# Performance work log

Measured on AMD Instinct MI355X. Metric: run time of the kernel, lower is better.

## Reference

```python
import jax, jax.numpy as jnp
import numpy as np

N = 50000       # nodes
E = 800000      # edges (before self-loops)
NFEAT = 256
NHID = 64
NHEADS = 4
NOUT = 256
NEG_SLOPE = 0.2
BN_EPS = 1e-5
LN_EPS = 1e-5


def setup_inputs() -> dict:
    key = jax.random.key(0)
    ks = jax.random.split(key, 12)
    g = lambda k, s: (jax.random.normal(k, s, dtype=jnp.float32) * 0.05)
    inp = {
        "x": jax.random.normal(ks[0], (N, NFEAT), dtype=jnp.float32),
        "edge_index": jax.random.randint(ks[1], (2, E), 0, N, dtype=jnp.int32),
        # layer 1: GATConv(NFEAT, NHID, heads=NHEADS, concat=True)
        "W1": g(ks[2], (NFEAT, NHEADS * NHID)),
        "att_src1": g(ks[3], (NHEADS, NHID)),
        "att_dst1": g(ks[4], (NHEADS, NHID)),
        "bias1": jnp.zeros((NHEADS * NHID,), jnp.float32),
        # layer 2: GATConv(NHEADS*NHID, NOUT, heads=1, concat=False)
        "W2": g(ks[5], (NHEADS * NHID, NOUT)),
        "att_src2": g(ks[6], (1, NOUT)),
        "att_dst2": g(ks[7], (1, NOUT)),
        "bias2": jnp.zeros((NOUT,), jnp.float32),
        # BatchNorm1d (eval mode: running stats)
        "bn_gamma": jnp.ones((NOUT,), jnp.float32),
        "bn_beta": jnp.zeros((NOUT,), jnp.float32),
        "bn_mean": g(ks[8], (NOUT,)),
        "bn_var": jnp.ones((NOUT,), jnp.float32),
        # LayerNorm
        "ln_gamma": jnp.ones((NOUT,), jnp.float32),
        "ln_beta": jnp.zeros((NOUT,), jnp.float32),
    }
    return inp


def _gat_conv(x, edge_index, W, att_src, att_dst, bias, concat):
    """PyG-style GATConv (eval mode, add_self_loops=True)."""
    n = x.shape[0]
    H, C = att_src.shape
    xp = (x @ W).reshape(n, H, C)                    # [N,H,C]
    loop = jnp.arange(n, dtype=edge_index.dtype)
    src = jnp.concatenate([edge_index[0], loop])     # message source j
    dst = jnp.concatenate([edge_index[1], loop])     # aggregation target i
    a_src = jnp.einsum("nhc,hc->nh", xp, att_src)    # [N,H]
    a_dst = jnp.einsum("nhc,hc->nh", xp, att_dst)
    e = jax.nn.leaky_relu(a_src[src] + a_dst[dst], NEG_SLOPE)  # [Etot,H]
    # segment softmax over edges sharing the same dst
    m = jax.ops.segment_max(e, dst, num_segments=n)
    e = jnp.exp(e - m[dst])
    denom = jax.ops.segment_sum(e, dst, num_segments=n)
    alpha = e / (denom[dst] + 1e-16)                 # [Etot,H]
    out = jax.ops.segment_sum(alpha[:, :, None] * xp[src], dst, num_segments=n)  # [N,H,C]
    out = out.reshape(n, H * C) if concat else out.mean(axis=1)
    return out + bias


def reference(x, edge_index, W1, att_src1, att_dst1, bias1,
              W2, att_src2, att_dst2, bias2,
              bn_gamma, bn_beta, bn_mean, bn_var, ln_gamma, ln_beta):
    # eval mode: F.dropout is identity
    h = jax.nn.elu(_gat_conv(x, edge_index, W1, att_src1, att_dst1, bias1, True))
    h = jax.nn.elu(_gat_conv(h, edge_index, W2, att_src2, att_dst2, bias2, False))
    # BatchNorm1d (eval: running stats)
    h = (h - bn_mean) * jax.lax.rsqrt(bn_var + BN_EPS) * bn_gamma + bn_beta
    # LayerNorm over last dim
    mu = h.mean(axis=-1, keepdims=True)
    var = jnp.mean((h - mu) ** 2, axis=-1, keepdims=True)
    h = (h - mu) * jax.lax.rsqrt(var + LN_EPS) * ln_gamma + ln_beta
    return h
```

## Files before the change

kernel.cpp:

```cpp
#include <hip/hip_runtime.h>
#include <cstddef>
#include <cstdint>

#define NNODES 50000
#define NEDGES 800000
#define FDIM   256

#define SCAN_BLOCKS 256
#define SCAN_CHUNK  ((NNODES + SCAN_BLOCKS - 1) / SCAN_BLOCKS)

typedef __attribute__((ext_vector_type(8))) _Float16 f16x8;
typedef __attribute__((ext_vector_type(8))) unsigned short ushort8;
typedef __attribute__((ext_vector_type(4))) float f32x4;

__device__ __forceinline__ float leaky_exp(float a) {
    float e = a > 0.f ? a : 0.2f * a;
    return __expf(e);
}
__device__ __forceinline__ unsigned short f2h(float f) {
    return __builtin_bit_cast(unsigned short, (_Float16)f);
}
__device__ __forceinline__ float hlo(uint32_t u) {
    _Float16 h = __builtin_bit_cast(_Float16, (unsigned short)(u & 0xffffu));
    return (float)h;
}
__device__ __forceinline__ float hhi(uint32_t u) {
    _Float16 h = __builtin_bit_cast(_Float16, (unsigned short)(u >> 16));
    return (float)h;
}
__device__ __forceinline__ float rlanef(float v, int l) {
    return __builtin_bit_cast(float,
        __builtin_amdgcn_readlane(__builtin_bit_cast(int, v), l));
}

__global__ __launch_bounds__(256) void cvt_k(const float* __restrict__ in,
                                             unsigned short* __restrict__ out,
                                             int n8) {
    int i = blockIdx.x * 256 + threadIdx.x;
    if (i >= n8) return;
    const float4* p = (const float4*)in + (size_t)i * 2;
    float4 a = p[0], b = p[1];
    ushort8 r;
    r[0] = f2h(a.x); r[1] = f2h(a.y); r[2] = f2h(a.z); r[3] = f2h(a.w);
    r[4] = f2h(b.x); r[5] = f2h(b.y); r[6] = f2h(b.z); r[7] = f2h(b.w);
    *(ushort8*)(out + (size_t)i * 8) = r;
}

__global__ __launch_bounds__(256) void wprep_k(const float* __restrict__ W,
                                               unsigned short* __restrict__ Wt) {
    int n = blockIdx.x, k = threadIdx.x;
    Wt[n * 256 + k] = f2h(W[k * 256 + n]);
}

__global__ __launch_bounds__(256) void gemm_mfma(const unsigned short* __restrict__ A,
                                                 const unsigned short* __restrict__ Bt,
                                                 unsigned short* __restrict__ C, int M) {
    __shared__ unsigned short As[128 * 64];
    __shared__ unsigned short Bs[128 * 64];
    const int t = threadIdx.x;
    const int lane = t & 63, wid = t >> 6;
    const int wr = wid >> 1, wc = wid & 1;
    const int bm = blockIdx.x * 128;
    const int bn = blockIdx.y * 128;
    f32x4 acc[4][4] = {};
    const int lrow = t >> 3, lslot = t & 7;
    for (int k0 = 0; k0 < 256; k0 += 64) {
        __syncthreads();
#pragma unroll
        for (int i = 0; i < 4; ++i) {
            int row = lrow + 32 * i;
            int ga = bm + row; ga = ga < M ? ga : M - 1;
            uint4 av = *(const uint4*)(A + (size_t)ga * FDIM + k0 + lslot * 8);
            *(uint4*)(As + row * 64 + ((lslot ^ (row & 7)) << 3)) = av;
            uint4 bv = *(const uint4*)(Bt + (size_t)(bn + row) * FDIM + k0 + lslot * 8);
            *(uint4*)(Bs + row * 64 + ((lslot ^ (row & 7)) << 3)) = bv;
        }
        __syncthreads();
#pragma unroll
        for (int ks = 0; ks < 2; ++ks) {
            const int kq = ks * 4 + (lane >> 4);
            f16x8 a[4], b[4];
#pragma unroll
            for (int f = 0; f < 4; ++f) {
                int ra = wr * 64 + f * 16 + (lane & 15);
                a[f] = *(const f16x8*)(As + ra * 64 + ((kq ^ (ra & 7)) << 3));
                int rb = wc * 64 + f * 16 + (lane & 15);
                b[f] = *(const f16x8*)(Bs + rb * 64 + ((kq ^ (rb & 7)) << 3));
            }
#pragma unroll
            for (int mf = 0; mf < 4; ++mf)
#pragma unroll
                for (int nf = 0; nf < 4; ++nf)
                    acc[mf][nf] = __builtin_amdgcn_mfma_f32_16x16x32_f16(
                        a[mf], b[nf], acc[mf][nf], 0, 0, 0);
        }
    }
    const int col0 = bn + wc * 64 + (lane & 15);
    const int row00 = bm + wr * 64 + (lane >> 4) * 4;
#pragma unroll
    for (int mf = 0; mf < 4; ++mf)
#pragma unroll
        for (int nf = 0; nf < 4; ++nf) {
            f32x4 v = acc[mf][nf];
            int col = col0 + nf * 16;
#pragma unroll
            for (int r = 0; r < 4; ++r) {
                int row = row00 + mf * 16 + r;
                if (row < M) C[(size_t)row * FDIM + col] = f2h(v[r]);
            }
        }
}

template <int H>
__global__ __launch_bounds__(256) void aprep_k(const unsigned short* __restrict__ xp,
                                               const float* __restrict__ atts,
                                               const float* __restrict__ attd,
                                               float* __restrict__ as_,
                                               float* __restrict__ ad_) {
    const int lane = threadIdx.x & 63;
    const int n = blockIdx.x * 4 + (threadIdx.x >> 6);
    if (n >= NNODES) return;
    const int c = lane << 2;
    uint2 u = *(const uint2*)(xp + (size_t)n * FDIM + c);
    float v0 = hlo(u.x), v1 = hhi(u.x), v2 = hlo(u.y), v3 = hhi(u.y);
    float4 s4 = *(const float4*)(atts + c);
    float4 d4 = *(const float4*)(attd + c);
    float ss = v0 * s4.x + v1 * s4.y + v2 * s4.z + v3 * s4.w;
    float sd = v0 * d4.x + v1 * d4.y + v2 * d4.z + v3 * d4.w;
    constexpr int G = 64 / H;
#pragma unroll
    for (int off = 1; off < G; off <<= 1) {
        ss += __shfl_xor(ss, off);
        sd += __shfl_xor(sd, off);
    }
    if ((lane & (G - 1)) == 0) {
        int h = lane / G;
        as_[n * H + h] = ss;
        ad_[n * H + h] = sd;
    }
}

__global__ __launch_bounds__(256) void hist_k(const int* __restrict__ ei,
                                              int* __restrict__ deg) {
    int e = blockIdx.x * 256 + threadIdx.x;
    if (e < NEDGES) atomicAdd(&deg[ei[NEDGES + e]], 1);
}

__global__ __launch_bounds__(256) void scanA_k(const int* __restrict__ deg,
                                               int* __restrict__ bsum) {
    const int b = blockIdx.x, t = threadIdx.x;
    const int i = b * SCAN_CHUNK + t;
    int v = (t < SCAN_CHUNK && i < NNODES) ? deg[i] : 0;
#pragma unroll
    for (int off = 1; off < 64; off <<= 1) v += __shfl_xor(v, off);
    __shared__ int ws[4];
    if ((t & 63) == 0) ws[t >> 6] = v;
    __syncthreads();
    if (t == 0) bsum[b] = ws[0] + ws[1] + ws[2] + ws[3];
}

__global__ __launch_bounds__(256) void scanB_k(const int* __restrict__ bsum,
                                               int* __restrict__ boff,
                                               int* __restrict__ rowptr) {
    const int t = threadIdx.x;
    const int lane = t & 63, wid = t >> 6;
    int orig = bsum[t];
    int v = orig;
#pragma unroll
    for (int off = 1; off < 64; off <<= 1) {
        int u = __shfl_up(v, off);
        if (lane >= off) v += u;
    }
    __shared__ int ws[4], wo[4];
    if (lane == 63) ws[wid] = v;
    __syncthreads();
    if (t == 0) {
        int a = 0;
        for (int k = 0; k < 4; ++k) { wo[k] = a; a += ws[k]; }
        rowptr[NNODES] = a;
    }
    __syncthreads();
    boff[t] = wo[wid] + v - orig;
}

__global__ __launch_bounds__(256) void scanC_k(const int* __restrict__ deg,
                                               const int* __restrict__ boff,
                                               int* __restrict__ rowptr) {
    const int b = blockIdx.x, t = threadIdx.x;
    const int i = b * SCAN_CHUNK + t;
    const bool ok = (t < SCAN_CHUNK && i < NNODES);
    int orig = ok ? deg[i] : 0;
    int v = orig;
    const int lane = t & 63, wid = t >> 6;
#pragma unroll
    for (int off = 1; off < 64; off <<= 1) {
        int u = __shfl_up(v, off);
        if (lane >= off) v += u;
    }
    __shared__ int ws[4], wo[4];
    if (lane == 63) ws[wid] = v;
    __syncthreads();
    if (t == 0) {
        int a = 0;
        for (int k = 0; k < 4; ++k) { wo[k] = a; a += ws[k]; }
    }
    __syncthreads();
    if (ok) rowptr[i] = boff[b] + wo[wid] + v - orig;
}

__global__ __launch_bounds__(256) void scatter_k(const int* __restrict__ ei,
                                                 const int* __restrict__ rowptr,
                                                 int* __restrict__ deg,
                                                 int* __restrict__ ssrc) {
    int e = blockIdx.x * 256 + threadIdx.x;
    if (e >= NEDGES) return;
    int s = ei[e], d = ei[NEDGES + e];
    int old = atomicSub(&deg[d], 1);
    ssrc[rowptr[d + 1] - old] = s;
}

__global__ __launch_bounds__(256) void gather1_k(const unsigned short* __restrict__ xp,
                                                 const float* __restrict__ as_,
                                                 const float* __restrict__ ad_,
                                                 const int* __restrict__ rowptr,
                                                 const int* __restrict__ ssrc,
                                                 const float* __restrict__ bias,
                                                 unsigned short* __restrict__ out) {
    const int lane = threadIdx.x & 63;
    const int n = blockIdx.x * 4 + (threadIdx.x >> 6);
    if (n >= NNODES) return;
    const int h = lane >> 4;
    const int c = lane << 2;
    const int eloc = lane >> 2;
    const int hh = lane & 3;
    const float adW = ad_[n * 4 + hh];
    float a0 = 0.f, a1 = 0.f, a2 = 0.f, a3 = 0.f, den = 0.f;
    const int beg = rowptr[n], end = rowptr[n + 1];
    for (int base = beg; base < end; base += 16) {
        int my_e = base + eloc;
        float wv = 0.f; int sv = 0;
        if (my_e < end) {
            sv = ssrc[my_e];
            wv = leaky_exp(as_[sv * 4 + hh] + adW);
        }
        float dred = wv;
#pragma unroll
        for (int off = 4; off < 64; off <<= 1) dred += __shfl_xor(dred, off);
        den += __shfl(dred, h);
        const int cnt = min(16, end - base);
        int e = 0;
        for (; e + 8 <= cnt; e += 8) {
            uint2 u[8]; float w[8];
#pragma unroll
            for (int q = 0; q < 8; ++q) {
                int sq = __builtin_amdgcn_readlane(sv, (e + q) << 2);
                u[q] = *(const uint2*)(xp + (((unsigned)sq << 8) + (unsigned)c));
                w[q] = __shfl(wv, ((e + q) << 2) | h);
            }
#pragma unroll
            for (int q = 0; q < 8; ++q) {
                a0 = fmaf(hlo(u[q].x), w[q], a0);
                a1 = fmaf(hhi(u[q].x), w[q], a1);
                a2 = fmaf(hlo(u[q].y), w[q], a2);
                a3 = fmaf(hhi(u[q].y), w[q], a3);
            }
        }
        for (; e < cnt; ++e) {
            int sq = __builtin_amdgcn_readlane(sv, e << 2);
            uint2 u0 = *(const uint2*)(xp + (((unsigned)sq << 8) + (unsigned)c));
            float w0 = __shfl(wv, (e << 2) | h);
            a0 = fmaf(hlo(u0.x), w0, a0); a1 = fmaf(hhi(u0.x), w0, a1);
            a2 = fmaf(hlo(u0.y), w0, a2); a3 = fmaf(hhi(u0.y), w0, a3);
        }
    }
    {
        float w = leaky_exp(as_[n * 4 + h] + ad_[n * 4 + h]);
        uint2 u = *(const uint2*)(xp + (((unsigned)n << 8) + (unsigned)c));
        a0 = fmaf(hlo(u.x), w, a0); a1 = fmaf(hhi(u.x), w, a1);
        a2 = fmaf(hlo(u.y), w, a2); a3 = fmaf(hhi(u.y), w, a3);
        den += w;
    }
    const float inv = 1.f / (den + 1e-16f);
    float4 b4 = *(const float4*)(bias + c);
    float o[4] = {a0 * inv + b4.x, a1 * inv + b4.y,
                  a2 * inv + b4.z, a3 * inv + b4.w};
#pragma unroll
    for (int j = 0; j < 4; ++j) o[j] = o[j] > 0.f ? o[j] : __expf(o[j]) - 1.f;
    ushort4 r;
    r.x = f2h(o[0]); r.y = f2h(o[1]); r.z = f2h(o[2]); r.w = f2h(o[3]);
    *(ushort4*)(out + (size_t)n * FDIM + c) = r;
}

__global__ __launch_bounds__(256) void gather2_k(const unsigned short* __restrict__ xp,
                                                 const float* __restrict__ as_,
                                                 const float* __restrict__ ad_,
                                                 const int* __restrict__ rowptr,
                                                 const int* __restrict__ ssrc,
                                                 const float* __restrict__ bias,
                                                 const float* __restrict__ bng,
                                                 const float* __restrict__ bnb,
                                                 const float* __restrict__ bnm,
                                                 const float* __restrict__ bnv,
                                                 const float* __restrict__ lng,
                                                 const float* __restrict__ lnb,
                                                 float* __restrict__ out) {
    const int lane = threadIdx.x & 63;
    const int n = blockIdx.x * 4 + (threadIdx.x >> 6);
    if (n >= NNODES) return;
    const int c = lane << 2;
    const float adn = ad_[n];
    float a0 = 0.f, a1 = 0.f, a2 = 0.f, a3 = 0.f, den = 0.f;
    const int beg = rowptr[n], end = rowptr[n + 1];
    for (int base = beg; base < end; base += 64) {
        int my_e = base + lane;
        float wv = 0.f; int sv = 0;
        if (my_e < end) {
            sv = ssrc[my_e];
            wv = leaky_exp(as_[sv] + adn);
        }
        float dred = wv;
#pragma unroll
        for (int off = 1; off < 64; off <<= 1) dred += __shfl_xor(dred, off);
        den += dred;
        const int cnt = min(64, end - base);
        int e = 0;
        for (; e + 8 <= cnt; e += 8) {
            uint2 u[8]; float w[8];
#pragma unroll
            for (int q = 0; q < 8; ++q) {
                int sq = __builtin_amdgcn_readlane(sv, e + q);
                u[q] = *(const uint2*)(xp + (((unsigned)sq << 8) + (unsigned)c));
                w[q] = rlanef(wv, e + q);
            }
#pragma unroll
            for (int q = 0; q < 8; ++q) {
                a0 = fmaf(hlo(u[q].x), w[q], a0);
                a1 = fmaf(hhi(u[q].x), w[q], a1);
                a2 = fmaf(hlo(u[q].y), w[q], a2);
                a3 = fmaf(hhi(u[q].y), w[q], a3);
            }
        }
        for (; e < cnt; ++e) {
            int sq = __builtin_amdgcn_readlane(sv, e);
            uint2 u0 = *(const uint2*)(xp + (((unsigned)sq << 8) + (unsigned)c));
            float w0 = rlanef(wv, e);
            a0 = fmaf(hlo(u0.x), w0, a0); a1 = fmaf(hhi(u0.x), w0, a1);
            a2 = fmaf(hlo(u0.y), w0, a2); a3 = fmaf(hhi(u0.y), w0, a3);
        }
    }
    {
        float w = leaky_exp(as_[n] + adn);
        uint2 u = *(const uint2*)(xp + (((unsigned)n << 8) + (unsigned)c));
        a0 = fmaf(hlo(u.x), w, a0); a1 = fmaf(hhi(u.x), w, a1);
        a2 = fmaf(hlo(u.y), w, a2); a3 = fmaf(hhi(u.y), w, a3);
        den += w;
    }
    const float inv = 1.f / (den + 1e-16f);
    float vals[4] = {a0 * inv, a1 * inv, a2 * inv, a3 * inv};
#pragma unroll
    for (int j = 0; j < 4; ++j) {
        float o = vals[j] + bias[c + j];
        o = o > 0.f ? o : __expf(o) - 1.f;
        o = (o - bnm[c + j]) * rsqrtf(bnv[c + j] + 1e-5f) * bng[c + j]
            + bnb[c + j];
        vals[j] = o;
    }
    float s1 = vals[0] + vals[1] + vals[2] + vals[3];
    float s2 = vals[0] * vals[0] + vals[1] * vals[1] +
               vals[2] * vals[2] + vals[3] * vals[3];
#pragma unroll
    for (int off = 1; off < 64; off <<= 1) {
        s1 += __shfl_xor(s1, off);
        s2 += __shfl_xor(s2, off);
    }
    float mu  = s1 * (1.f / 256.f);
    float var = s2 * (1.f / 256.f) - mu * mu;
    float r   = rsqrtf(var + 1e-5f);
#pragma unroll
    for (int j = 0; j < 4; ++j)
        out[(size_t)n * FDIM + c + j] = (vals[j] - mu) * r * lng[c + j] + lnb[c + j];
}

extern "C" void kernel_launch(void* const* d_in, const int* in_sizes, int n_in,
                              void* d_out, int out_size, void* d_ws, size_t ws_size,
                              hipStream_t stream) {
    const float* x      = (const float*)d_in[0];
    const int*   ei     = (const int*)d_in[1];
    const float* W1     = (const float*)d_in[2];
    const float* atts1  = (const float*)d_in[3];
    const float* attd1  = (const float*)d_in[4];
    const float* bias1  = (const float*)d_in[5];
    const float* W2     = (const float*)d_in[6];
    const float* atts2  = (const float*)d_in[7];
    const float* attd2  = (const float*)d_in[8];
    const float* bias2  = (const float*)d_in[9];
    const float* bng    = (const float*)d_in[10];
    const float* bnb    = (const float*)d_in[11];
    const float* bnm    = (const float*)d_in[12];
    const float* bnv    = (const float*)d_in[13];
    const float* lng    = (const float*)d_in[14];
    const float* lnb    = (const float*)d_in[15];

    const size_t NF = (size_t)NNODES * FDIM;
    unsigned short* xpbf = (unsigned short*)d_ws;
    unsigned short* xbf  = xpbf + NF;
    unsigned short* wt1  = xbf + NF;
    unsigned short* wt2  = wt1 + 65536;
    float* as1   = (float*)(wt2 + 65536);
    float* ad1   = as1 + (size_t)NNODES * 4;
    float* as2   = ad1 + (size_t)NNODES * 4;
    float* ad2   = as2 + NNODES;
    int*   deg    = (int*)(ad2 + NNODES);
    int*   rowptr = deg + NNODES;
    int*   bsum   = rowptr + (NNODES + 1);
    int*   boff   = bsum + SCAN_BLOCKS;
    int*   ssrc   = boff + SCAN_BLOCKS;
    float* outf  = (float*)d_out;

    const dim3 gemm_grid((NNODES + 127) / 128, 2);
    const int node_wave_blocks = (NNODES + 3) / 4;
    const int edge_thread_blocks = (NEDGES + 255) / 256;
    const int cvt_blocks = (int)((NF / 8 + 255) / 256);

    cvt_k<<<cvt_blocks, 256, 0, stream>>>(x, xbf, (int)(NF / 8));
    wprep_k<<<256, 256, 0, stream>>>(W1, wt1);
    wprep_k<<<256, 256, 0, stream>>>(W2, wt2);
    hipMemsetAsync(deg, 0, NNODES * sizeof(int), stream);
    hist_k<<<edge_thread_blocks, 256, 0, stream>>>(ei, deg);
    scanA_k<<<SCAN_BLOCKS, 256, 0, stream>>>(deg, bsum);
    scanB_k<<<1, 256, 0, stream>>>(bsum, boff, rowptr);
    scanC_k<<<SCAN_BLOCKS, 256, 0, stream>>>(deg, boff, rowptr);
    scatter_k<<<edge_thread_blocks, 256, 0, stream>>>(ei, rowptr, deg, ssrc);

    gemm_mfma<<<gemm_grid, 256, 0, stream>>>(xbf, wt1, xpbf, NNODES);
    aprep_k<4><<<node_wave_blocks, 256, 0, stream>>>(xpbf, atts1, attd1, as1, ad1);
    gather1_k<<<node_wave_blocks, 256, 0, stream>>>(xpbf, as1, ad1, rowptr, ssrc,
                                                    bias1, xbf);

    gemm_mfma<<<gemm_grid, 256, 0, stream>>>(xbf, wt2, xpbf, NNODES);
    aprep_k<1><<<node_wave_blocks, 256, 0, stream>>>(xpbf, atts2, attd2, as2, ad2);
    gather2_k<<<node_wave_blocks, 256, 0, stream>>>(xpbf, as2, ad2, rowptr, ssrc,
                                                    bias2, bng, bnb, bnm, bnv,
                                                    lng, lnb, outf);
}
```

Measured before the change: 286.5 us.

## Fuse fp32 conversion and attention logits into full-width MFMA GEMM

Removes the separate fp32-to-fp16 conversion pass by converting x tiles while loading them inside the first GEMM. It also drops the aprep kernels by computing the attention source/destination dot products from the fp32 accumulators in the GEMM epilogue, accumulated with atomics into buffers zeroed by a memset. The GEMM now covers all 256 output columns per block with 512 threads instead of two column blocks, and the weight transpose goes through a coalesced shared-memory tile. The trade-offs are extra atomics, larger shared memory, and a different rounding of the logits, which now come from fp32 values instead of fp16.

```diff
diff --git a/kernel.cpp b/kernel.cpp
--- a/kernel.cpp
+++ b/kernel.cpp
@@ -33,47 +33,84 @@
         __builtin_amdgcn_readlane(__builtin_bit_cast(int, v), l));
 }
 
-__global__ __launch_bounds__(256) void cvt_k(const float* __restrict__ in,
-                                             unsigned short* __restrict__ out,
-                                             int n8) {
-    int i = blockIdx.x * 256 + threadIdx.x;
-    if (i >= n8) return;
-    const float4* p = (const float4*)in + (size_t)i * 2;
-    float4 a = p[0], b = p[1];
-    ushort8 r;
-    r[0] = f2h(a.x); r[1] = f2h(a.y); r[2] = f2h(a.z); r[3] = f2h(a.w);
-    r[4] = f2h(b.x); r[5] = f2h(b.y); r[6] = f2h(b.z); r[7] = f2h(b.w);
-    *(ushort8*)(out + (size_t)i * 8) = r;
-}
-
 __global__ __launch_bounds__(256) void wprep_k(const float* __restrict__ W,
                                                unsigned short* __restrict__ Wt) {
-    int n = blockIdx.x, k = threadIdx.x;
-    Wt[n * 256 + k] = f2h(W[k * 256 + n]);
-}
-
-__global__ __launch_bounds__(256) void gemm_mfma(const unsigned short* __restrict__ A,
-                                                 const unsigned short* __restrict__ Bt,
-                                                 unsigned short* __restrict__ C, int M) {
+    __shared__ unsigned short tile[64][68];
+    const int kb = blockIdx.x * 64, nb = blockIdx.y * 64;
+    const int t = threadIdx.x;
+    const int kk = t >> 2, ns = (t & 3) * 16;
+    const float* src = W + (size_t)(kb + kk) * 256 + nb + ns;
+#pragma unroll
+    for (int j = 0; j < 16; j += 4) {
+        float4 f = *(const float4*)(src + j);
+        tile[kk][ns + j + 0] = f2h(f.x);
+        tile[kk][ns + j + 1] = f2h(f.y);
+        tile[kk][ns + j + 2] = f2h(f.z);
+        tile[kk][ns + j + 3] = f2h(f.w);
+    }
+    __syncthreads();
+    const int nn = t >> 2, ks = (t & 3) * 16;
+    ushort8 r0, r1;
+#pragma unroll
+    for (int j = 0; j < 8; ++j) {
+        r0[j] = tile[ks + j][nn];
+        r1[j] = tile[ks + 8 + j][nn];
+    }
+    unsigned short* dst = Wt + (size_t)(nb + nn) * 256 + kb + ks;
+    *(ushort8*)(dst + 0) = r0;
+    *(ushort8*)(dst + 8) = r1;
+}
+
+template <bool AFP32, int H>
+__global__ __launch_bounds__(512) void gemm_fused(const void* __restrict__ Aab,
+                                                  const unsigned short* __restrict__ Bt,
+                                                  unsigned short* __restrict__ C,
+                                                  const float* __restrict__ atts,
+                                                  const float* __restrict__ attd,
+                                                  float* __restrict__ as_,
+                                                  float* __restrict__ ad_,
+                                                  int M) {
     __shared__ unsigned short As[128 * 64];
-    __shared__ unsigned short Bs[128 * 64];
+    __shared__ unsigned short Bs[256 * 64];
     const int t = threadIdx.x;
     const int lane = t & 63, wid = t >> 6;
-    const int wr = wid >> 1, wc = wid & 1;
+    const int wr = wid >> 2, wc = wid & 3;
     const int bm = blockIdx.x * 128;
-    const int bn = blockIdx.y * 128;
     f32x4 acc[4][4] = {};
-    const int lrow = t >> 3, lslot = t & 7;
+    const int arow = t >> 2, asub = t & 3;
+    const int brow = t >> 1, bsub = t & 1;
     for (int k0 = 0; k0 < 256; k0 += 64) {
         __syncthreads();
-#pragma unroll
-        for (int i = 0; i < 4; ++i) {
-            int row = lrow + 32 * i;
-            int ga = bm + row; ga = ga < M ? ga : M - 1;
-            uint4 av = *(const uint4*)(A + (size_t)ga * FDIM + k0 + lslot * 8);
-            *(uint4*)(As + row * 64 + ((lslot ^ (row & 7)) << 3)) = av;
-            uint4 bv = *(const uint4*)(Bt + (size_t)(bn + row) * FDIM + k0 + lslot * 8);
-            *(uint4*)(Bs + row * 64 + ((lslot ^ (row & 7)) << 3)) = bv;
+        {
+            int ga = bm + arow; ga = ga < M ? ga : M - 1;
+            if (AFP32) {
+                const float* A32 = (const float*)Aab;
+#pragma unroll
+                for (int s2 = 0; s2 < 2; ++s2) {
+                    int slot = asub * 2 + s2;
+                    const float* p = A32 + (size_t)ga * 256 + k0 + slot * 8;
+                    float4 f0 = *(const float4*)p;
+                    float4 f1 = *(const float4*)(p + 4);
+                    ushort8 r;
+                    r[0] = f2h(f0.x); r[1] = f2h(f0.y); r[2] = f2h(f0.z); r[3] = f2h(f0.w);
+                    r[4] = f2h(f1.x); r[5] = f2h(f1.y); r[6] = f2h(f1.z); r[7] = f2h(f1.w);
+                    *(ushort8*)(As + arow * 64 + ((slot ^ (arow & 7)) << 3)) = r;
+                }
+            } else {
+                const unsigned short* A16 = (const unsigned short*)Aab;
+#pragma unroll
+                for (int s2 = 0; s2 < 2; ++s2) {
+                    int slot = asub * 2 + s2;
+                    uint4 v = *(const uint4*)(A16 + (size_t)ga * 256 + k0 + slot * 8);
+                    *(uint4*)(As + arow * 64 + ((slot ^ (arow & 7)) << 3)) = v;
+                }
+            }
+#pragma unroll
+            for (int s4 = 0; s4 < 4; ++s4) {
+                int slot = bsub * 4 + s4;
+                uint4 v = *(const uint4*)(Bt + (size_t)brow * 256 + k0 + slot * 8);
+                *(uint4*)(Bs + brow * 64 + ((slot ^ (brow & 7)) << 3)) = v;
+            }
         }
         __syncthreads();
 #pragma unroll
@@ -95,8 +132,37 @@
                         a[mf], b[nf], acc[mf][nf], 0, 0, 0);
         }
     }
-    const int col0 = bn + wc * 64 + (lane & 15);
+    const int col0 = wc * 64 + (lane & 15);
     const int row00 = bm + wr * 64 + (lane >> 4) * 4;
+    float sv[4], dv[4];
+#pragma unroll
+    for (int nf = 0; nf < 4; ++nf) {
+        sv[nf] = atts[col0 + nf * 16];
+        dv[nf] = attd[col0 + nf * 16];
+    }
+    const int hsel = (H == 4) ? wc : 0;
+#pragma unroll
+    for (int mf = 0; mf < 4; ++mf)
+#pragma unroll
+        for (int r = 0; r < 4; ++r) {
+            float ps = 0.f, pd = 0.f;
+#pragma unroll
+            for (int nf = 0; nf < 4; ++nf) {
+                float v = acc[mf][nf][r];
+                ps = fmaf(v, sv[nf], ps);
+                pd = fmaf(v, dv[nf], pd);
+            }
+#pragma unroll
+            for (int off = 1; off < 16; off <<= 1) {
+                ps += __shfl_xor(ps, off);
+                pd += __shfl_xor(pd, off);
+            }
+            int row = row00 + mf * 16 + r;
+            if ((lane & 15) == 0 && row < M) {
+                unsafeAtomicAdd(&as_[row * H + hsel], ps);
+                unsafeAtomicAdd(&ad_[row * H + hsel], pd);
+            }
+        }
 #pragma unroll
     for (int mf = 0; mf < 4; ++mf)
 #pragma unroll
@@ -109,35 +175,6 @@
                 if (row < M) C[(size_t)row * FDIM + col] = f2h(v[r]);
             }
         }
-}
-
-template <int H>
-__global__ __launch_bounds__(256) void aprep_k(const unsigned short* __restrict__ xp,
-                                               const float* __restrict__ atts,
-                                               const float* __restrict__ attd,
-                                               float* __restrict__ as_,
-                                               float* __restrict__ ad_) {
-    const int lane = threadIdx.x & 63;
-    const int n = blockIdx.x * 4 + (threadIdx.x >> 6);
-    if (n >= NNODES) return;
-    const int c = lane << 2;
-    uint2 u = *(const uint2*)(xp + (size_t)n * FDIM + c);
-    float v0 = hlo(u.x), v1 = hhi(u.x), v2 = hlo(u.y), v3 = hhi(u.y);
-    float4 s4 = *(const float4*)(atts + c);
-    float4 d4 = *(const float4*)(attd + c);
-    float ss = v0 * s4.x + v1 * s4.y + v2 * s4.z + v3 * s4.w;
-    float sd = v0 * d4.x + v1 * d4.y + v2 * d4.z + v3 * d4.w;
-    constexpr int G = 64 / H;
-#pragma unroll
-    for (int off = 1; off < G; off <<= 1) {
-        ss += __shfl_xor(ss, off);
-        sd += __shfl_xor(sd, off);
-    }
-    if ((lane & (G - 1)) == 0) {
-        int h = lane / G;
-        as_[n * H + h] = ss;
-        ad_[n * H + h] = sd;
-    }
 }
 
 __global__ __launch_bounds__(256) void hist_k(const int* __restrict__ ei,
@@ -417,28 +454,27 @@
     int*   ssrc   = boff + SCAN_BLOCKS;
     float* outf  = (float*)d_out;
 
-    const dim3 gemm_grid((NNODES + 127) / 128, 2);
+    const int gemm_blocks = (NNODES + 127) / 128;
     const int node_wave_blocks = (NNODES + 3) / 4;
     const int edge_thread_blocks = (NEDGES + 255) / 256;
-    const int cvt_blocks = (int)((NF / 8 + 255) / 256);
-
-    cvt_k<<<cvt_blocks, 256, 0, stream>>>(x, xbf, (int)(NF / 8));
-    wprep_k<<<256, 256, 0, stream>>>(W1, wt1);
-    wprep_k<<<256, 256, 0, stream>>>(W2, wt2);
+
+    wprep_k<<<dim3(4, 4), 256, 0, stream>>>(W1, wt1);
+    wprep_k<<<dim3(4, 4), 256, 0, stream>>>(W2, wt2);
     hipMemsetAsync(deg, 0, NNODES * sizeof(int), stream);
+    hipMemsetAsync(as1, 0, (size_t)NNODES * 10 * sizeof(float), stream);
     hist_k<<<edge_thread_blocks, 256, 0, stream>>>(ei, deg);
     scanA_k<<<SCAN_BLOCKS, 256, 0, stream>>>(deg, bsum);
     scanB_k<<<1, 256, 0, stream>>>(bsum, boff, rowptr);
     scanC_k<<<SCAN_BLOCKS, 256, 0, stream>>>(deg, boff, rowptr);
     scatter_k<<<edge_thread_blocks, 256, 0, stream>>>(ei, rowptr, deg, ssrc);
 
-    gemm_mfma<<<gemm_grid, 256, 0, stream>>>(xbf, wt1, xpbf, NNODES);
-    aprep_k<4><<<node_wave_blocks, 256, 0, stream>>>(xpbf, atts1, attd1, as1, ad1);
+    gemm_fused<true, 4><<<gemm_blocks, 512, 0, stream>>>(
+        x, wt1, xpbf, atts1, attd1, as1, ad1, NNODES);
     gather1_k<<<node_wave_blocks, 256, 0, stream>>>(xpbf, as1, ad1, rowptr, ssrc,
                                                     bias1, xbf);
 
-    gemm_mfma<<<gemm_grid, 256, 0, stream>>>(xbf, wt2, xpbf, NNODES);
-    aprep_k<1><<<node_wave_blocks, 256, 0, stream>>>(xpbf, atts2, attd2, as2, ad2);
+    gemm_fused<false, 1><<<gemm_blocks, 512, 0, stream>>>(
+        xbf, wt2, xpbf, atts2, attd2, as2, ad2, NNODES);
     gather2_k<<<node_wave_blocks, 256, 0, stream>>>(xpbf, as2, ad2, rowptr, ssrc,
                                                     bias2, bng, bnb, bnm, bnv,
                                                     lng, lnb, outf);
```

Result: slower. 293.3 us (+2.4%).

## Split wavefront into two half-waves processing alternate edges with 16-byte row loads

Applied to the files above, without the earlier changes.

Both gather kernels now have each half of a 64-lane wavefront handle a different edge. Each lane loads 8 fp16 features (uint4) instead of 4, and the two halves' partial sums are combined with a cross-half shuffle at the end. The next chunk's source indices and attention logits are prefetched one iteration ahead, and the epilogue parameters and outputs use vectorized float4 loads and stores. This is meant to raise memory-level parallelism and load width on the irregular gathers, at the cost of more registers, a final reduction, and half the lanes idling during the epilogue.

```diff
diff --git a/kernel.cpp b/kernel.cpp
--- a/kernel.cpp
+++ b/kernel.cpp
@@ -27,10 +27,6 @@
 __device__ __forceinline__ float hhi(uint32_t u) {
     _Float16 h = __builtin_bit_cast(_Float16, (unsigned short)(u >> 16));
     return (float)h;
-}
-__device__ __forceinline__ float rlanef(float v, int l) {
-    return __builtin_bit_cast(float,
-        __builtin_amdgcn_readlane(__builtin_bit_cast(int, v), l));
 }
 
 __global__ __launch_bounds__(256) void cvt_k(const float* __restrict__ in,
@@ -229,19 +225,27 @@
     const int lane = threadIdx.x & 63;
     const int n = blockIdx.x * 4 + (threadIdx.x >> 6);
     if (n >= NNODES) return;
-    const int h = lane >> 4;
-    const int c = lane << 2;
+    const int half = lane >> 5;
+    const int fl = lane & 31;
+    const int c = fl << 3;
+    const int h = fl >> 3;
     const int eloc = lane >> 2;
     const int hh = lane & 3;
     const float adW = ad_[n * 4 + hh];
-    float a0 = 0.f, a1 = 0.f, a2 = 0.f, a3 = 0.f, den = 0.f;
+    float a[8] = {};
+    float den = 0.f;
     const int beg = rowptr[n], end = rowptr[n + 1];
+    int sv = 0; float av = 0.f;
+    {
+        int e0 = beg + eloc;
+        if (e0 < end) { sv = ssrc[e0]; av = as_[sv * 4 + hh]; }
+    }
     for (int base = beg; base < end; base += 16) {
-        int my_e = base + eloc;
-        float wv = 0.f; int sv = 0;
-        if (my_e < end) {
-            sv = ssrc[my_e];
-            wv = leaky_exp(as_[sv * 4 + hh] + adW);
+        float wv = (base + eloc < end) ? leaky_exp(av + adW) : 0.f;
+        int sv_n = 0; float av_n = 0.f;
+        {
+            int nx = base + 16 + eloc;
+            if (nx < end) { sv_n = ssrc[nx]; av_n = as_[sv_n * 4 + hh]; }
         }
         float dred = wv;
 #pragma unroll
@@ -250,45 +254,67 @@
         const int cnt = min(16, end - base);
         int e = 0;
         for (; e + 8 <= cnt; e += 8) {
-            uint2 u[8]; float w[8];
-#pragma unroll
-            for (int q = 0; q < 8; ++q) {
-                int sq = __builtin_amdgcn_readlane(sv, (e + q) << 2);
-                u[q] = *(const uint2*)(xp + (((unsigned)sq << 8) + (unsigned)c));
-                w[q] = __shfl(wv, ((e + q) << 2) | h);
-            }
-#pragma unroll
-            for (int q = 0; q < 8; ++q) {
-                a0 = fmaf(hlo(u[q].x), w[q], a0);
-                a1 = fmaf(hhi(u[q].x), w[q], a1);
-                a2 = fmaf(hlo(u[q].y), w[q], a2);
-                a3 = fmaf(hhi(u[q].y), w[q], a3);
-            }
-        }
-        for (; e < cnt; ++e) {
-            int sq = __builtin_amdgcn_readlane(sv, e << 2);
-            uint2 u0 = *(const uint2*)(xp + (((unsigned)sq << 8) + (unsigned)c));
-            float w0 = __shfl(wv, (e << 2) | h);
-            a0 = fmaf(hlo(u0.x), w0, a0); a1 = fmaf(hhi(u0.x), w0, a1);
-            a2 = fmaf(hlo(u0.y), w0, a2); a3 = fmaf(hhi(u0.y), w0, a3);
-        }
-    }
+            uint4 u[4]; float w[4];
+#pragma unroll
+            for (int q = 0; q < 4; ++q) {
+                int idx = e + 2 * q + half;
+                int sq = __shfl(sv, idx << 2);
+                w[q] = __shfl(wv, (idx << 2) | h);
+                u[q] = *(const uint4*)(xp + (((unsigned)sq << 8) + (unsigned)c));
+            }
+#pragma unroll
+            for (int q = 0; q < 4; ++q) {
+                a[0] = fmaf(hlo(u[q].x), w[q], a[0]);
+                a[1] = fmaf(hhi(u[q].x), w[q], a[1]);
+                a[2] = fmaf(hlo(u[q].y), w[q], a[2]);
+                a[3] = fmaf(hhi(u[q].y), w[q], a[3]);
+                a[4] = fmaf(hlo(u[q].z), w[q], a[4]);
+                a[5] = fmaf(hhi(u[q].z), w[q], a[5]);
+                a[6] = fmaf(hlo(u[q].w), w[q], a[6]);
+                a[7] = fmaf(hhi(u[q].w), w[q], a[7]);
+            }
+        }
+        for (; e < cnt; e += 2) {
+            int idx = e + half;
+            int sq = __shfl(sv, idx << 2);
+            float w0 = __shfl(wv, (idx << 2) | h);
+            if (idx < cnt) {
+                uint4 u0 = *(const uint4*)(xp + (((unsigned)sq << 8) + (unsigned)c));
+                a[0] = fmaf(hlo(u0.x), w0, a[0]); a[1] = fmaf(hhi(u0.x), w0, a[1]);
+                a[2] = fmaf(hlo(u0.y), w0, a[2]); a[3] = fmaf(hhi(u0.y), w0, a[3]);
+                a[4] = fmaf(hlo(u0.z), w0, a[4]); a[5] = fmaf(hhi(u0.z), w0, a[5]);
+                a[6] = fmaf(hlo(u0.w), w0, a[6]); a[7] = fmaf(hhi(u0.w), w0, a[7]);
+            }
+        }
+        sv = sv_n; av = av_n;
+    }
+#pragma unroll
+    for (int j = 0; j < 8; ++j) a[j] += __shfl_xor(a[j], 32);
     {
         float w = leaky_exp(as_[n * 4 + h] + ad_[n * 4 + h]);
-        uint2 u = *(const uint2*)(xp + (((unsigned)n << 8) + (unsigned)c));
-        a0 = fmaf(hlo(u.x), w, a0); a1 = fmaf(hhi(u.x), w, a1);
-        a2 = fmaf(hlo(u.y), w, a2); a3 = fmaf(hhi(u.y), w, a3);
+        uint4 u = *(const uint4*)(xp + (((unsigned)n << 8) + (unsigned)c));
+        a[0] = fmaf(hlo(u.x), w, a[0]); a[1] = fmaf(hhi(u.x), w, a[1]);
+        a[2] = fmaf(hlo(u.y), w, a[2]); a[3] = fmaf(hhi(u.y), w, a[3]);
+        a[4] = fmaf(hlo(u.z), w, a[4]); a[5] = fmaf(hhi(u.z), w, a[5]);
+        a[6] = fmaf(hlo(u.w), w, a[6]); a[7] = fmaf(hhi(u.w), w, a[7]);
         den += w;
     }
-    const float inv = 1.f / (den + 1e-16f);
-    float4 b4 = *(const float4*)(bias + c);
-    float o[4] = {a0 * inv + b4.x, a1 * inv + b4.y,
-                  a2 * inv + b4.z, a3 * inv + b4.w};
-#pragma unroll
-    for (int j = 0; j < 4; ++j) o[j] = o[j] > 0.f ? o[j] : __expf(o[j]) - 1.f;
-    ushort4 r;
-    r.x = f2h(o[0]); r.y = f2h(o[1]); r.z = f2h(o[2]); r.w = f2h(o[3]);
-    *(ushort4*)(out + (size_t)n * FDIM + c) = r;
+    if (lane < 32) {
+        const float inv = 1.f / (den + 1e-16f);
+        float4 b0 = *(const float4*)(bias + c);
+        float4 b1 = *(const float4*)(bias + c + 4);
+        float o[8] = {a[0] * inv + b0.x, a[1] * inv + b0.y,
+                      a[2] * inv + b0.z, a[3] * inv + b0.w,
+                      a[4] * inv + b1.x, a[5] * inv + b1.y,
+                      a[6] * inv + b1.z, a[7] * inv + b1.w};
+        ushort8 r;
+#pragma unroll
+        for (int j = 0; j < 8; ++j) {
+            float v = o[j] > 0.f ? o[j] : __expf(o[j]) - 1.f;
+            r[j] = f2h(v);
+        }
+        *(ushort8*)(out + (size_t)n * FDIM + c) = r;
+    }
 }
 
 __global__ __launch_bounds__(256) void gather2_k(const unsigned short* __restrict__ xp,
@@ -307,16 +333,24 @@
     const int lane = threadIdx.x & 63;
     const int n = blockIdx.x * 4 + (threadIdx.x >> 6);
     if (n >= NNODES) return;
-    const int c = lane << 2;
+    const int half = lane >> 5;
+    const int fl = lane & 31;
+    const int c = fl << 3;
     const float adn = ad_[n];
-    float a0 = 0.f, a1 = 0.f, a2 = 0.f, a3 = 0.f, den = 0.f;
+    float a[8] = {};
+    float den = 0.f;
     const int beg = rowptr[n], end = rowptr[n + 1];
+    int sv = 0; float av = 0.f;
+    {
+        int e0 = beg + lane;
+        if (e0 < end) { sv = ssrc[e0]; av = as_[sv]; }
+    }
     for (int base = beg; base < end; base += 64) {
-        int my_e = base + lane;
-        float wv = 0.f; int sv = 0;
-        if (my_e < end) {
-            sv = ssrc[my_e];
-            wv = leaky_exp(as_[sv] + adn);
+        float wv = (base + lane < end) ? leaky_exp(av + adn) : 0.f;
+        int sv_n = 0; float av_n = 0.f;
+        {
+            int nx = base + 64 + lane;
+            if (nx < end) { sv_n = ssrc[nx]; av_n = as_[sv_n]; }
         }
         float dred = wv;
 #pragma unroll
@@ -325,60 +359,98 @@
         const int cnt = min(64, end - base);
         int e = 0;
         for (; e + 8 <= cnt; e += 8) {
-            uint2 u[8]; float w[8];
-#pragma unroll
-            for (int q = 0; q < 8; ++q) {
-                int sq = __builtin_amdgcn_readlane(sv, e + q);
-                u[q] = *(const uint2*)(xp + (((unsigned)sq << 8) + (unsigned)c));
-                w[q] = rlanef(wv, e + q);
-            }
-#pragma unroll
-            for (int q = 0; q < 8; ++q) {
-                a0 = fmaf(hlo(u[q].x), w[q], a0);
-                a1 = fmaf(hhi(u[q].x), w[q], a1);
-                a2 = fmaf(hlo(u[q].y), w[q], a2);
-                a3 = fmaf(hhi(u[q].y), w[q], a3);
-            }
-        }
-        for (; e < cnt; ++e) {
-            int sq = __builtin_amdgcn_readlane(sv, e);
-            uint2 u0 = *(const uint2*)(xp + (((unsigned)sq << 8) + (unsigned)c));
-            float w0 = rlanef(wv, e);
-            a0 = fmaf(hlo(u0.x), w0, a0); a1 = fmaf(hhi(u0.x), w0, a1);
-            a2 = fmaf(hlo(u0.y), w0, a2); a3 = fmaf(hhi(u0.y), w0, a3);
-        }
-    }
+            uint4 u[4]; float w[4];
+#pragma unroll
+            for (int q = 0; q < 4; ++q) {
+                int idx = e + 2 * q + half;
+                int sq = __shfl(sv, idx);
+                w[q] = __shfl(wv, idx);
+                u[q] = *(const uint4*)(xp + (((unsigned)sq << 8) + (unsigned)c));
+            }
+#pragma unroll
+            for (int q = 0; q < 4; ++q) {
+                a[0] = fmaf(hlo(u[q].x), w[q], a[0]);
+                a[1] = fmaf(hhi(u[q].x), w[q], a[1]);
+                a[2] = fmaf(hlo(u[q].y), w[q], a[2]);
+                a[3] = fmaf(hhi(u[q].y), w[q], a[3]);
+                a[4] = fmaf(hlo(u[q].z), w[q], a[4]);
+                a[5] = fmaf(hhi(u[q].z), w[q], a[5]);
+                a[6] = fmaf(hlo(u[q].w), w[q], a[6]);
+                a[7] = fmaf(hhi(u[q].w), w[q], a[7]);
+            }
+        }
+        for (; e < cnt; e += 2) {
+            int idx = e + half;
+            int sq = __shfl(sv, idx);
+            float w0 = __shfl(wv, idx);
+            if (idx < cnt) {
+                uint4 u0 = *(const uint4*)(xp + (((unsigned)sq << 8) + (unsigned)c));
+                a[0] = fmaf(hlo(u0.x), w0, a[0]); a[1] = fmaf(hhi(u0.x), w0, a[1]);
+                a[2] = fmaf(hlo(u0.y), w0, a[2]); a[3] = fmaf(hhi(u0.y), w0, a[3]);
+                a[4] = fmaf(hlo(u0.z), w0, a[4]); a[5] = fmaf(hhi(u0.z), w0, a[5]);
+                a[6] = fmaf(hlo(u0.w), w0, a[6]); a[7] = fmaf(hhi(u0.w), w0, a[7]);
+            }
+        }
+        sv = sv_n; av = av_n;
+    }
+#pragma unroll
+    for (int j = 0; j < 8; ++j) a[j] += __shfl_xor(a[j], 32);
     {
         float w = leaky_exp(as_[n] + adn);
-        uint2 u = *(const uint2*)(xp + (((unsigned)n << 8) + (unsigned)c));
-        a0 = fmaf(hlo(u.x), w, a0); a1 = fmaf(hhi(u.x), w, a1);
-        a2 = fmaf(hlo(u.y), w, a2); a3 = fmaf(hhi(u.y), w, a3);
+        uint4 u = *(const uint4*)(xp + (((unsigned)n << 8) + (unsigned)c));
+        a[0] = fmaf(hlo(u.x), w, a[0]); a[1] = fmaf(hhi(u.x), w, a[1]);
+        a[2] = fmaf(hlo(u.y), w, a[2]); a[3] = fmaf(hhi(u.y), w, a[3]);
+        a[4] = fmaf(hlo(u.z), w, a[4]); a[5] = fmaf(hhi(u.z), w, a[5]);
+        a[6] = fmaf(hlo(u.w), w, a[6]); a[7] = fmaf(hhi(u.w), w, a[7]);
         den += w;
     }
     const float inv = 1.f / (den + 1e-16f);
-    float vals[4] = {a0 * inv, a1 * inv, a2 * inv, a3 * inv};
-#pragma unroll
-    for (int j = 0; j < 4; ++j) {
-        float o = vals[j] + bias[c + j];
+    float vals[8];
+    float4 bb0 = *(const float4*)(bias + c), bb1 = *(const float4*)(bias + c + 4);
+    float4 bm0 = *(const float4*)(bnm + c),  bm1 = *(const float4*)(bnm + c + 4);
+    float4 bv0 = *(const float4*)(bnv + c),  bv1 = *(const float4*)(bnv + c + 4);
+    float4 bg0 = *(const float4*)(bng + c),  bg1 = *(const float4*)(bng + c + 4);
+    float4 be0 = *(const float4*)(bnb + c),  be1 = *(const float4*)(bnb + c + 4);
+    float bbv[8] = {bb0.x, bb0.y, bb0.z, bb0.w, bb1.x, bb1.y, bb1.z, bb1.w};
+    float bmv[8] = {bm0.x, bm0.y, bm0.z, bm0.w, bm1.x, bm1.y, bm1.z, bm1.w};
+    float bvv[8] = {bv0.x, bv0.y, bv0.z, bv0.w, bv1.x, bv1.y, bv1.z, bv1.w};
+    float bgv[8] = {bg0.x, bg0.y, bg0.z, bg0.w, bg1.x, bg1.y, bg1.z, bg1.w};
+    float bev[8] = {be0.x, be0.y, be0.z, be0.w, be1.x, be1.y, be1.z, be1.w};
+#pragma unroll
+    for (int j = 0; j < 8; ++j) {
+        float o = a[j] * inv + bbv[j];
         o = o > 0.f ? o : __expf(o) - 1.f;
-        o = (o - bnm[c + j]) * rsqrtf(bnv[c + j] + 1e-5f) * bng[c + j]
-            + bnb[c + j];
+        o = (o - bmv[j]) * rsqrtf(bvv[j] + 1e-5f) * bgv[j] + bev[j];
         vals[j] = o;
     }
-    float s1 = vals[0] + vals[1] + vals[2] + vals[3];
-    float s2 = vals[0] * vals[0] + vals[1] * vals[1] +
-               vals[2] * vals[2] + vals[3] * vals[3];
-#pragma unroll
-    for (int off = 1; off < 64; off <<= 1) {
+    float s1 = 0.f, s2 = 0.f;
+#pragma unroll
+    for (int j = 0; j < 8; ++j) { s1 += vals[j]; s2 += vals[j] * vals[j]; }
+#pragma unroll
+    for (int off = 1; off < 32; off <<= 1) {
         s1 += __shfl_xor(s1, off);
         s2 += __shfl_xor(s2, off);
     }
-    float mu  = s1 * (1.f / 256.f);
-    float var = s2 * (1.f / 256.f) - mu * mu;
-    float r   = rsqrtf(var + 1e-5f);
-#pragma unroll
-    for (int j = 0; j < 4; ++j)
-        out[(size_t)n * FDIM + c + j] = (vals[j] - mu) * r * lng[c + j] + lnb[c + j];
+    if (lane < 32) {
+        float mu  = s1 * (1.f / 256.f);
+        float var = s2 * (1.f / 256.f) - mu * mu;
+        float r   = rsqrtf(var + 1e-5f);
+        float4 lg0 = *(const float4*)(lng + c), lg1 = *(const float4*)(lng + c + 4);
+        float4 lb0 = *(const float4*)(lnb + c), lb1 = *(const float4*)(lnb + c + 4);
+        float lgv[8] = {lg0.x, lg0.y, lg0.z, lg0.w, lg1.x, lg1.y, lg1.z, lg1.w};
+        float lbv[8] = {lb0.x, lb0.y, lb0.z, lb0.w, lb1.x, lb1.y, lb1.z, lb1.w};
+        float4 o0, o1;
+        o0.x = (vals[0] - mu) * r * lgv[0] + lbv[0];
+        o0.y = (vals[1] - mu) * r * lgv[1] + lbv[1];
+        o0.z = (vals[2] - mu) * r * lgv[2] + lbv[2];
+        o0.w = (vals[3] - mu) * r * lgv[3] + lbv[3];
+        o1.x = (vals[4] - mu) * r * lgv[4] + lbv[4];
+        o1.y = (vals[5] - mu) * r * lgv[5] + lbv[5];
+        o1.z = (vals[6] - mu) * r * lgv[6] + lbv[6];
+        o1.w = (vals[7] - mu) * r * lgv[7] + lbv[7];
+        *(float4*)(out + (size_t)n * FDIM + c) = o0;
+        *(float4*)(out + (size_t)n * FDIM + c + 4) = o1;
+    }
 }
 
 extern "C" void kernel_launch(void* const* d_in, const int* in_sizes, int n_in,
```

Result: no change. 291.8 us (+1.8%).

## Fuse fp32-to-fp16 input conversion and layer-1 attention logits into GEMM

Applied to the files above, without the earlier changes.

The first GEMM now reads the fp32 input directly and converts it to fp16 while staging into shared memory, which removes the separate cvt kernel and its fp16 round trip through memory. Its epilogue also computes the per-head source and destination attention logits from the fp32 accumulators with a 16-lane shuffle reduction, replacing the aprep_k<4> pass that re-read the projected features. The two weight-transpose launches are merged into one 2D grid. The GEMM now loads twice the A bytes from global memory and carries extra epilogue work. The logits come from fp32 accumulators rather than fp16-rounded outputs, so they differ slightly from before.

```diff
diff --git a/kernel.cpp b/kernel.cpp
--- a/kernel.cpp
+++ b/kernel.cpp
@@ -33,35 +33,33 @@
         __builtin_amdgcn_readlane(__builtin_bit_cast(int, v), l));
 }
 
-__global__ __launch_bounds__(256) void cvt_k(const float* __restrict__ in,
-                                             unsigned short* __restrict__ out,
-                                             int n8) {
-    int i = blockIdx.x * 256 + threadIdx.x;
-    if (i >= n8) return;
-    const float4* p = (const float4*)in + (size_t)i * 2;
-    float4 a = p[0], b = p[1];
-    ushort8 r;
-    r[0] = f2h(a.x); r[1] = f2h(a.y); r[2] = f2h(a.z); r[3] = f2h(a.w);
-    r[4] = f2h(b.x); r[5] = f2h(b.y); r[6] = f2h(b.z); r[7] = f2h(b.w);
-    *(ushort8*)(out + (size_t)i * 8) = r;
-}
-
-__global__ __launch_bounds__(256) void wprep_k(const float* __restrict__ W,
-                                               unsigned short* __restrict__ Wt) {
+__global__ __launch_bounds__(256) void wprep_k(const float* __restrict__ W1,
+                                               unsigned short* __restrict__ Wt1,
+                                               const float* __restrict__ W2,
+                                               unsigned short* __restrict__ Wt2) {
+    const float* W = blockIdx.y ? W2 : W1;
+    unsigned short* Wt = blockIdx.y ? Wt2 : Wt1;
     int n = blockIdx.x, k = threadIdx.x;
     Wt[n * 256 + k] = f2h(W[k * 256 + n]);
 }
 
-__global__ __launch_bounds__(256) void gemm_mfma(const unsigned short* __restrict__ A,
+template <bool AFP32, bool FUSE_LOGITS>
+__global__ __launch_bounds__(256) void gemm_mfma(const void* __restrict__ Aab,
                                                  const unsigned short* __restrict__ Bt,
-                                                 unsigned short* __restrict__ C, int M) {
+                                                 unsigned short* __restrict__ C,
+                                                 const float* __restrict__ atts,
+                                                 const float* __restrict__ attd,
+                                                 float* __restrict__ as_,
+                                                 float* __restrict__ ad_,
+                                                 int M) {
     __shared__ unsigned short As[128 * 64];
     __shared__ unsigned short Bs[128 * 64];
     const int t = threadIdx.x;
     const int lane = t & 63, wid = t >> 6;
     const int wr = wid >> 1, wc = wid & 1;
     const int bm = blockIdx.x * 128;
-    const int bn = blockIdx.y * 128;
+    const int bny = blockIdx.y;
+    const int bn = bny * 128;
     f32x4 acc[4][4] = {};
     const int lrow = t >> 3, lslot = t & 7;
     for (int k0 = 0; k0 < 256; k0 += 64) {
@@ -70,8 +68,19 @@
         for (int i = 0; i < 4; ++i) {
             int row = lrow + 32 * i;
             int ga = bm + row; ga = ga < M ? ga : M - 1;
-            uint4 av = *(const uint4*)(A + (size_t)ga * FDIM + k0 + lslot * 8);
-            *(uint4*)(As + row * 64 + ((lslot ^ (row & 7)) << 3)) = av;
+            if (AFP32) {
+                const float* p = (const float*)Aab + (size_t)ga * FDIM + k0 + lslot * 8;
+                float4 f0 = *(const float4*)p;
+                float4 f1 = *(const float4*)(p + 4);
+                ushort8 r;
+                r[0] = f2h(f0.x); r[1] = f2h(f0.y); r[2] = f2h(f0.z); r[3] = f2h(f0.w);
+                r[4] = f2h(f1.x); r[5] = f2h(f1.y); r[6] = f2h(f1.z); r[7] = f2h(f1.w);
+                *(ushort8*)(As + row * 64 + ((lslot ^ (row & 7)) << 3)) = r;
+            } else {
+                const unsigned short* A16 = (const unsigned short*)Aab;
+                uint4 av = *(const uint4*)(A16 + (size_t)ga * FDIM + k0 + lslot * 8);
+                *(uint4*)(As + row * 64 + ((lslot ^ (row & 7)) << 3)) = av;
+            }
             uint4 bv = *(const uint4*)(Bt + (size_t)(bn + row) * FDIM + k0 + lslot * 8);
             *(uint4*)(Bs + row * 64 + ((lslot ^ (row & 7)) << 3)) = bv;
         }
@@ -97,6 +106,37 @@
     }
     const int col0 = bn + wc * 64 + (lane & 15);
     const int row00 = bm + wr * 64 + (lane >> 4) * 4;
+    if (FUSE_LOGITS) {
+        const int head = 2 * bny + wc;
+        float sv4[4], dv4[4];
+#pragma unroll
+        for (int nf = 0; nf < 4; ++nf) {
+            sv4[nf] = atts[col0 + nf * 16];
+            dv4[nf] = attd[col0 + nf * 16];
+        }
+#pragma unroll
+        for (int mf = 0; mf < 4; ++mf)
+#pragma unroll
+            for (int r = 0; r < 4; ++r) {
+                float ps = 0.f, pd = 0.f;
+#pragma unroll
+                for (int nf = 0; nf < 4; ++nf) {
+                    float v = acc[mf][nf][r];
+                    ps = fmaf(v, sv4[nf], ps);
+                    pd = fmaf(v, dv4[nf], pd);
+                }
+#pragma unroll
+                for (int off = 1; off < 16; off <<= 1) {
+                    ps += __shfl_xor(ps, off);
+                    pd += __shfl_xor(pd, off);
+                }
+                int row = row00 + mf * 16 + r;
+                if ((lane & 15) == 0 && row < M) {
+                    as_[row * 4 + head] = ps;
+                    ad_[row * 4 + head] = pd;
+                }
+            }
+    }
 #pragma unroll
     for (int mf = 0; mf < 4; ++mf)
 #pragma unroll
@@ -420,11 +460,8 @@
     const dim3 gemm_grid((NNODES + 127) / 128, 2);
     const int node_wave_blocks = (NNODES + 3) / 4;
     const int edge_thread_blocks = (NEDGES + 255) / 256;
-    const int cvt_blocks = (int)((NF / 8 + 255) / 256);
-
-    cvt_k<<<cvt_blocks, 256, 0, stream>>>(x, xbf, (int)(NF / 8));
-    wprep_k<<<256, 256, 0, stream>>>(W1, wt1);
-    wprep_k<<<256, 256, 0, stream>>>(W2, wt2);
+
+    wprep_k<<<dim3(256, 2), 256, 0, stream>>>(W1, wt1, W2, wt2);
     hipMemsetAsync(deg, 0, NNODES * sizeof(int), stream);
     hist_k<<<edge_thread_blocks, 256, 0, stream>>>(ei, deg);
     scanA_k<<<SCAN_BLOCKS, 256, 0, stream>>>(deg, bsum);
@@ -432,12 +469,13 @@
     scanC_k<<<SCAN_BLOCKS, 256, 0, stream>>>(deg, boff, rowptr);
     scatter_k<<<edge_thread_blocks, 256, 0, stream>>>(ei, rowptr, deg, ssrc);
 
-    gemm_mfma<<<gemm_grid, 256, 0, stream>>>(xbf, wt1, xpbf, NNODES);
-    aprep_k<4><<<node_wave_blocks, 256, 0, stream>>>(xpbf, atts1, attd1, as1, ad1);
+    gemm_mfma<true, true><<<gemm_grid, 256, 0, stream>>>(
+        x, wt1, xpbf, atts1, attd1, as1, ad1, NNODES);
     gather1_k<<<node_wave_blocks, 256, 0, stream>>>(xpbf, as1, ad1, rowptr, ssrc,
                                                     bias1, xbf);
 
-    gemm_mfma<<<gemm_grid, 256, 0, stream>>>(xbf, wt2, xpbf, NNODES);
+    gemm_mfma<false, false><<<gemm_grid, 256, 0, stream>>>(
+        xbf, wt2, xpbf, nullptr, nullptr, nullptr, nullptr, NNODES);
     aprep_k<1><<<node_wave_blocks, 256, 0, stream>>>(xpbf, atts2, attd2, as2, ad2);
     gather2_k<<<node_wave_blocks, 256, 0, stream>>>(xpbf, as2, ad2, rowptr, ssrc,
                                                     bias2, bng, bnb, bnm, bnv,
```

After: 290.8 us. Within noise of the previous version (+1.5%).
